# Kernel tuning notes

Hardware: AMD Instinct MI355X
Metric: run time of the kernel (lower is better)

## Reference

```python
import jax, jax.numpy as jnp
import numpy as np

H = 128          # hidden_dim
B = 4096         # number of graphs (segments)
N = 1048576      # total nodes
NUM_OBS = 1


def setup_inputs() -> dict:
    key = jax.random.key(0)
    ks = jax.random.split(key, 10)
    h = jax.random.normal(ks[0], (N, H), dtype=jnp.float32)
    batch = jnp.sort(jax.random.randint(ks[1], (N,), 0, B, dtype=jnp.int64))
    s = 1.0 / np.sqrt(H)
    s2 = 1.0 / np.sqrt(2 * H)
    # gate: Linear(H,H) -> tanh -> Linear(H,1)
    gate_w1 = jax.random.uniform(ks[2], (H, H), jnp.float32, -s, s)
    gate_b1 = jax.random.uniform(ks[3], (H,), jnp.float32, -s, s)
    gate_w2 = jax.random.uniform(ks[4], (H, 1), jnp.float32, -s, s)
    gate_b2 = jax.random.uniform(ks[5], (1,), jnp.float32, -s, s)
    # mlp: Linear(2H,H) -> ReLU -> Linear(H,num_obs)  (dropout off in eval)
    mlp_w1 = jax.random.uniform(ks[6], (2 * H, H), jnp.float32, -s2, s2)
    mlp_b1 = jax.random.uniform(ks[7], (H,), jnp.float32, -s2, s2)
    mlp_w2 = jax.random.uniform(ks[8], (H, NUM_OBS), jnp.float32, -s, s)
    mlp_b2 = jax.random.uniform(ks[9], (NUM_OBS,), jnp.float32, -s, s)
    return {"h": h, "batch": batch,
            "gate_w1": gate_w1, "gate_b1": gate_b1,
            "gate_w2": gate_w2, "gate_b2": gate_b2,
            "mlp_w1": mlp_w1, "mlp_b1": mlp_b1,
            "mlp_w2": mlp_w2, "mlp_b2": mlp_b2}


def reference(h, batch, gate_w1, gate_b1, gate_w2, gate_b2,
              mlp_w1, mlp_b1, mlp_w2, mlp_b2):
    # gate scores per node: (N,)
    score = (jnp.tanh(h @ gate_w1 + gate_b1) @ gate_w2 + gate_b2)[:, 0]
    # segment softmax over nodes of each graph (numerically stable)
    seg_max = jax.ops.segment_max(score, batch, num_segments=B)
    e = jnp.exp(score - seg_max[batch])
    seg_sum = jax.ops.segment_sum(e, batch, num_segments=B)
    attn = e / seg_sum[batch]                      # (N,)
    # attention-weighted sum pooling: (B, H)
    g_attn = jax.ops.segment_sum(h * attn[:, None], batch, num_segments=B)
    # max pooling: (B, H)
    g_max = jax.ops.segment_max(h, batch, num_segments=B)
    g = jnp.concatenate([g_attn, g_max], axis=-1)  # (B, 2H)
    hidden = jax.nn.relu(g @ mlp_w1 + mlp_b1)
    return hidden @ mlp_w2 + mlp_b2               # (B, NUM_OBS)
```

## Files before the change

### kernel.cpp

```cpp
#include <hip/hip_runtime.h>
#include <hip/hip_bf16.h>
#include <cfloat>

#define HD 128

typedef float f32x4 __attribute__((ext_vector_type(4)));
typedef __bf16 bf16x8 __attribute__((ext_vector_type(8)));

__global__ void seg_bounds_kernel(const int* __restrict__ batch, int n, int nseg,
                                  int* __restrict__ seg_start) {
  int b = blockIdx.x * blockDim.x + threadIdx.x;
  if (b > nseg) return;
  if (b == nseg) { seg_start[b] = n; return; }
  int lo = 0, hi = n;
  while (lo < hi) {
    int mid = (lo + hi) >> 1;
    if (batch[mid] < b) lo = mid + 1; else hi = mid;
  }
  seg_start[b] = lo;
}

template <int CTRL>
__device__ __forceinline__ float dpp_ror(float v) {
  return __int_as_float(__builtin_amdgcn_update_dpp(
      0, __float_as_int(v), CTRL, 0xF, 0xF, true));
}


#define LOAD_TILE(BUF, T)                                                   \
  {                                                                         \
    const int nIt_ = (T) * 16 + lr;                                         \
    const size_t row_ = (size_t)s0 + (size_t)min(nIt_, lenm1);              \
    const float* hp_ = h + row_ * HD + 8 * kl;                              \
    _Pragma("unroll")                                                       \
    for (int kt = 0; kt < 4; ++kt) {                                        \
      *reinterpret_cast<float4*>(&BUF[8 * kt]) =                            \
          *reinterpret_cast<const float4*>(hp_ + 32 * kt);                  \
      *reinterpret_cast<float4*>(&BUF[8 * kt + 4]) =                        \
          *reinterpret_cast<const float4*>(hp_ + 32 * kt + 4);              \
    }                                                                       \
  }

#define PROC_TILE(BUF, T)                                                   \
  {                                                                         \
    const bool valid_ = ((T) * 16 + lr) < len;                              \
                 \
    asm volatile("" : "+v"(Cb));                                            \
    float p2_[4] = {0.f, 0.f, 0.f, 0.f};                                    \
    _Pragma("unroll")                                                       \
    for (int hf = 0; hf < 2; ++hf) {                                        \
      f32x4 macc_[4];                                                       \
      _Pragma("unroll")                                                     \
      for (int fh = 0; fh < 4; ++fh) macc_[fh] = (f32x4){0.f, 0.f, 0.f, 0.f}; \
      __builtin_amdgcn_s_setprio(1);                                        \
      _Pragma("unroll")                                                     \
      for (int kt = 0; kt < 4; ++kt) {                                      \
        bf16x8 acur_;                                                       \
        _Pragma("unroll")                                                   \
        for (int j = 0; j < 8; ++j) acur_[j] = (__bf16)BUF[8 * kt + j];     \
        const char* bp_ = reinterpret_cast<const char*>(sWt) +              \
                          (Cb + ((kt ^ hi2) << 6)) + hf * 16384;            \
        bf16x8 bfr_[4];                                                     \
        _Pragma("unroll")                                                   \
        for (int fh = 0; fh < 4; ++fh)                                      \
          bfr_[fh] = *reinterpret_cast<const bf16x8*>(bp_ + fh * 4096);     \
        _Pragma("unroll")                                                   \
        for (int fh = 0; fh < 4; ++fh)                                      \
          macc_[fh] = __builtin_amdgcn_mfma_f32_16x16x32_bf16(              \
              acur_, bfr_[fh], macc_[fh], 0, 0, 0);                         \
      }                                                                     \
      __builtin_amdgcn_s_setprio(0);                                        \
      _Pragma("unroll")                                                     \
      for (int fh = 0; fh < 4; ++fh) {                                      \
        const int f_ = 4 * hf + fh;                                         \
        _Pragma("unroll")                                                   \
        for (int r = 0; r < 4; ++r) {                                       \
          const float xe_ = fmaf(LOG2E2, macc_[fh][r], b1s[f_]);            \
          const float e_ = exp2f(xe_);                                      \
          const float t_ = __builtin_amdgcn_rcpf(1.f + e_);                 \
          p2_[r] = fmaf(t_, w2r[f_], p2_[r]);                               \
        }                                                                   \
      }                                                                     \
    }                                                                       \
               \
    _Pragma("unroll")                                                       \
    for (int r = 0; r < 4; ++r) {                                           \
      p2_[r] += dpp_ror<0x121>(p2_[r]);                                     \
      p2_[r] += dpp_ror<0x122>(p2_[r]);                                     \
      p2_[r] += dpp_ror<0x124>(p2_[r]);                                     \
      p2_[r] += dpp_ror<0x128>(p2_[r]);                                     \
    }                                                                       \
    const int rr_ = lr & 3;                                                 \
    const float psel_ =                                                     \
        rr_ == 0 ? p2_[0] : (rr_ == 1 ? p2_[1] : (rr_ == 2 ? p2_[2]         \
                                                            : p2_[3]));     \
    const float sc_ = __shfl(psel_, ((lr >> 2) << 4) | (lr & 3), 64);       \
    const float w_ = valid_ ? exp2f(sc_ * NEG2LOG2E) : 0.f;                 \
    s += w_;                                                                \
    _Pragma("unroll")                                                       \
    for (int j = 0; j < 32; ++j) {                                          \
      acc[j] = fmaf(BUF[j], w_, acc[j]);                                    \
      gm[j] = fmaxf(gm[j], BUF[j]);                                         \
    }                                                                       \
  }

__global__ __launch_bounds__(256, 2) void fused_pool_kernel(
    const float* __restrict__ h, const float* __restrict__ w1,
    const float* __restrict__ b1, const float* __restrict__ w2,
    const int* __restrict__ seg_start, int B,
    const float* __restrict__ w1m, const float* __restrict__ b1m,
    const float* __restrict__ w2m, const float* __restrict__ b2m,
    float* __restrict__ out)
{
  __shared__ __bf16 sWt[HD * HD];
  __shared__ float sG[4][256];

  for (int i = threadIdx.x; i < HD * HD / 4; i += 256) {
    const int k = i >> 5;
    const int c4 = (i & 31) << 2;
    const float4 v = reinterpret_cast<const float4*>(w1)[i];
    const float vv[4] = {v.x, v.y, v.z, v.w};
#pragma unroll
    for (int q = 0; q < 4; ++q) {
      const int c = c4 + q;
      sWt[c * HD + ((((k >> 3) ^ (c & 15)) << 3) | (k & 7))] = (__bf16)vv[q];
    }
  }
  __syncthreads();

  const float LOG2E2    = 2.88539008177792681f;
  const float NEG2LOG2E = -2.88539008177792681f;

  const int lane = threadIdx.x & 63;
  const int wid  = threadIdx.x >> 6;
  const int lr   = lane & 15;
  const int kl   = lane >> 4;

  float w2r[8], b1s[8];
#pragma unroll
  for (int f = 0; f < 8; ++f) {
    w2r[f] = w2[16 * f + lr];
    b1s[f] = LOG2E2 * b1[16 * f + lr];
  }

  const int hi2 = (lr >> 2) & 3;
  int Cb = lr * 256 + ((kl ^ (lr & 3)) << 4);

  const int segStride = gridDim.x * 4;
  for (int b = blockIdx.x * 4 + wid; b < B; b += segStride) {
    const int s0  = seg_start[b];
    const int len = seg_start[b + 1] - s0;
    const int lenm1 = len - 1;
    const int nt  = (len + 15) >> 4;

    float s = 0.f;
    float acc[32], gm[32];
#pragma unroll
    for (int j = 0; j < 32; ++j) { acc[j] = 0.f; gm[j] = -FLT_MAX; }

    if (nt > 0) {
      float hA[32], hB[32];
      LOAD_TILE(hA, 0)
      LOAD_TILE(hB, 1)
      for (int t = 0; t < nt; t += 2) {
        PROC_TILE(hA, t)
        LOAD_TILE(hA, t + 2)
        PROC_TILE(hB, t + 1)
        LOAD_TILE(hB, t + 3)
      }
    }

#pragma unroll
    for (int st = 1; st <= 8; st <<= 1) {
      if (st == 1) {
        s += dpp_ror<0x121>(s);
#pragma unroll
        for (int j = 0; j < 32; ++j) {
          acc[j] += dpp_ror<0x121>(acc[j]);
          gm[j] = fmaxf(gm[j], dpp_ror<0x121>(gm[j]));
        }
      } else if (st == 2) {
        s += dpp_ror<0x122>(s);
#pragma unroll
        for (int j = 0; j < 32; ++j) {
          acc[j] += dpp_ror<0x122>(acc[j]);
          gm[j] = fmaxf(gm[j], dpp_ror<0x122>(gm[j]));
        }
      } else if (st == 4) {
        s += dpp_ror<0x124>(s);
#pragma unroll
        for (int j = 0; j < 32; ++j) {
          acc[j] += dpp_ror<0x124>(acc[j]);
          gm[j] = fmaxf(gm[j], dpp_ror<0x124>(gm[j]));
        }
      } else {
        s += dpp_ror<0x128>(s);
#pragma unroll
        for (int j = 0; j < 32; ++j) {
          acc[j] += dpp_ror<0x128>(acc[j]);
          gm[j] = fmaxf(gm[j], dpp_ror<0x128>(gm[j]));
        }
      }
    }

    if (lr == 0) {
      const float invS = (s > 0.f) ? 1.f / s : 0.f;
#pragma unroll
      for (int kt = 0; kt < 4; ++kt) {
        const int fb = 32 * kt + 8 * kl;
        float4 va, vb, ma, mb;
        va.x = acc[8*kt+0]*invS; va.y = acc[8*kt+1]*invS;
        va.z = acc[8*kt+2]*invS; va.w = acc[8*kt+3]*invS;
        vb.x = acc[8*kt+4]*invS; vb.y = acc[8*kt+5]*invS;
        vb.z = acc[8*kt+6]*invS; vb.w = acc[8*kt+7]*invS;
        ma.x = gm[8*kt+0]; ma.y = gm[8*kt+1]; ma.z = gm[8*kt+2]; ma.w = gm[8*kt+3];
        mb.x = gm[8*kt+4]; mb.y = gm[8*kt+5]; mb.z = gm[8*kt+6]; mb.w = gm[8*kt+7];
        *reinterpret_cast<float4*>(&sG[wid][fb])           = va;
        *reinterpret_cast<float4*>(&sG[wid][fb + 4])       = vb;
        *reinterpret_cast<float4*>(&sG[wid][128 + fb])     = ma;
        *reinterpret_cast<float4*>(&sG[wid][128 + fb + 4]) = mb;
      }
    }
    asm volatile("s_waitcnt lgkmcnt(0)" ::: "memory");

    {
      const int u = lane;
      float a0 = b1m[u], a1 = b1m[u + 64];
      const float* wp0 = w1m + u;
#pragma unroll 8
      for (int kq = 0; kq < 64; ++kq) {
        const float4 g4 = *reinterpret_cast<const float4*>(&sG[wid][4 * kq]);
        const float* wk = wp0 + (size_t)(4 * kq) * HD;
        a0 = fmaf(g4.x, wk[0],            a0);
        a1 = fmaf(g4.x, wk[64],           a1);
        a0 = fmaf(g4.y, wk[HD],           a0);
        a1 = fmaf(g4.y, wk[HD + 64],      a1);
        a0 = fmaf(g4.z, wk[2 * HD],       a0);
        a1 = fmaf(g4.z, wk[2 * HD + 64],  a1);
        a0 = fmaf(g4.w, wk[3 * HD],       a0);
        a1 = fmaf(g4.w, wk[3 * HD + 64],  a1);
      }
      float v = fmaxf(a0, 0.f) * w2m[u] + fmaxf(a1, 0.f) * w2m[u + 64];
#pragma unroll
      for (int off = 32; off >= 1; off >>= 1) v += __shfl_xor(v, off, 64);
      if (lane == 0) out[b] = v + b2m[0];
    }
  }
}

extern "C" void kernel_launch(void* const* d_in, const int* in_sizes, int n_in,
                              void* d_out, int out_size, void* d_ws, size_t ws_size,
                              hipStream_t stream) {
  const float* h       = (const float*)d_in[0];
  const int*   batch   = (const int*)d_in[1];
  const float* gate_w1 = (const float*)d_in[2];
  const float* gate_b1 = (const float*)d_in[3];
  const float* gate_w2 = (const float*)d_in[4];
  const float* mlp_w1  = (const float*)d_in[6];
  const float* mlp_b1  = (const float*)d_in[7];
  const float* mlp_w2  = (const float*)d_in[8];
  const float* mlp_b2  = (const float*)d_in[9];
  float* out = (float*)d_out;

  const int N = in_sizes[0] / HD;
  const int B = out_size;

  int* seg = (int*)d_ws;

  seg_bounds_kernel<<<(B + 256) / 256, 256, 0, stream>>>(batch, N, B, seg);
  fused_pool_kernel<<<1024, 256, 0, stream>>>(h, gate_w1, gate_b1, gate_w2,
                                              seg, B, mlp_w1, mlp_b1, mlp_w2,
                                              mlp_b2, out);
}
```

Baseline: 158.1 us.

## Triple-buffer node tiles as packed bf16 registers to deepen prefetch

Loads each 16-node tile into one fp32 staging buffer and immediately converts it to packed bf16 registers. This allows three tiles in flight (A/B/C rotation) instead of two fp32 buffers. The MFMA inputs, and also the attention-weighted sum and max pooling, now read the bf16 values. The goal is to cut register usage and hide more global-load latency, at the cost of reduced precision in the pooled outputs.

```diff
diff --git a/kernel.cpp b/kernel.cpp
--- a/kernel.cpp
+++ b/kernel.cpp
@@ -27,21 +27,32 @@
 }
 
 
-#define LOAD_TILE(BUF, T)                                                   \
+#define LOADF_TILE(T)                                                       \
   {                                                                         \
     const int nIt_ = (T) * 16 + lr;                                         \
     const size_t row_ = (size_t)s0 + (size_t)min(nIt_, lenm1);              \
     const float* hp_ = h + row_ * HD + 8 * kl;                              \
     _Pragma("unroll")                                                       \
     for (int kt = 0; kt < 4; ++kt) {                                        \
-      *reinterpret_cast<float4*>(&BUF[8 * kt]) =                            \
+      *reinterpret_cast<float4*>(&F[8 * kt]) =                              \
           *reinterpret_cast<const float4*>(hp_ + 32 * kt);                  \
-      *reinterpret_cast<float4*>(&BUF[8 * kt + 4]) =                        \
+      *reinterpret_cast<float4*>(&F[8 * kt + 4]) =                          \
           *reinterpret_cast<const float4*>(hp_ + 32 * kt + 4);              \
     }                                                                       \
   }
 
-#define PROC_TILE(BUF, T)                                                   \
+#define CVT_TILE(PK)                                                        \
+  {                                                                         \
+    _Pragma("unroll")                                                       \
+    for (int kt = 0; kt < 4; ++kt) {                                        \
+      bf16x8 p_;                                                            \
+      _Pragma("unroll")                                                     \
+      for (int j = 0; j < 8; ++j) p_[j] = (__bf16)F[8 * kt + j];            \
+      PK[kt] = p_;                                                          \
+    }                                                                       \
+  }
+
+#define PROC_TILE(PK, T)                                                    \
   {                                                                         \
     const bool valid_ = ((T) * 16 + lr) < len;                              \
                  \
@@ -55,9 +66,6 @@
       __builtin_amdgcn_s_setprio(1);                                        \
       _Pragma("unroll")                                                     \
       for (int kt = 0; kt < 4; ++kt) {                                      \
-        bf16x8 acur_;                                                       \
-        _Pragma("unroll")                                                   \
-        for (int j = 0; j < 8; ++j) acur_[j] = (__bf16)BUF[8 * kt + j];     \
         const char* bp_ = reinterpret_cast<const char*>(sWt) +              \
                           (Cb + ((kt ^ hi2) << 6)) + hf * 16384;            \
         bf16x8 bfr_[4];                                                     \
@@ -67,7 +75,7 @@
         _Pragma("unroll")                                                   \
         for (int fh = 0; fh < 4; ++fh)                                      \
           macc_[fh] = __builtin_amdgcn_mfma_f32_16x16x32_bf16(              \
-              acur_, bfr_[fh], macc_[fh], 0, 0, 0);                         \
+              PK[kt], bfr_[fh], macc_[fh], 0, 0, 0);                        \
       }                                                                     \
       __builtin_amdgcn_s_setprio(0);                                        \
       _Pragma("unroll")                                                     \
@@ -98,9 +106,13 @@
     const float w_ = valid_ ? exp2f(sc_ * NEG2LOG2E) : 0.f;                 \
     s += w_;                                                                \
     _Pragma("unroll")                                                       \
-    for (int j = 0; j < 32; ++j) {                                          \
-      acc[j] = fmaf(BUF[j], w_, acc[j]);                                    \
-      gm[j] = fmaxf(gm[j], BUF[j]);                                         \
+    for (int kt = 0; kt < 4; ++kt) {                                        \
+      _Pragma("unroll")                                                     \
+      for (int j = 0; j < 8; ++j) {                                         \
+        const float hv_ = (float)PK[kt][j];            \
+        acc[8 * kt + j] = fmaf(hv_, w_, acc[8 * kt + j]);                   \
+        gm[8 * kt + j] = fmaxf(gm[8 * kt + j], hv_);                        \
+      }                                                                     \
     }                                                                       \
   }
 
@@ -159,14 +171,21 @@
     for (int j = 0; j < 32; ++j) { acc[j] = 0.f; gm[j] = -FLT_MAX; }
 
     if (nt > 0) {
-      float hA[32], hB[32];
-      LOAD_TILE(hA, 0)
-      LOAD_TILE(hB, 1)
-      for (int t = 0; t < nt; t += 2) {
+      float F[32];
+      bf16x8 hA[4], hB[4], hC[4];
+      LOADF_TILE(0) CVT_TILE(hA)
+      LOADF_TILE(1) CVT_TILE(hB)
+      LOADF_TILE(2)
+      for (int t = 0; t < nt; t += 3) {
+        CVT_TILE(hC)
+        LOADF_TILE(t + 3)
         PROC_TILE(hA, t)
-        LOAD_TILE(hA, t + 2)
+        CVT_TILE(hA)
+        LOADF_TILE(t + 4)
         PROC_TILE(hB, t + 1)
-        LOAD_TILE(hB, t + 3)
+        CVT_TILE(hB)
+        LOADF_TILE(t + 5)
+        PROC_TILE(hC, t + 2)
       }
     }
 
```

Measured after the change: 355.0 us. +124.5%, slower.

## Stage h tiles into LDS via async global_load_lds with 4-deep ring

Applied to the files above, without the earlier changes.

Replaces the register double-buffered h loads with direct global-to-LDS async copies into a four-slot per-wave ring, prefetching four tiles ahead. The gate weight matrix is now held in registers (Bf fragments), so it no longer has to be read from LDS on every tile, which frees LDS for the staging buffers. Blocks shrink to 2 waves with 64KB of dynamic LDS and one block per CU, which lowers occupancy in exchange for deeper per-wave prefetch. The vmcnt/lgkmcnt bookkeeping is hand-tuned and fragile, and the large register footprint of the held weights may cause spills.

```diff
diff --git a/kernel.cpp b/kernel.cpp
--- a/kernel.cpp
+++ b/kernel.cpp
@@ -27,25 +27,47 @@
 }
 
 
-#define LOAD_TILE(BUF, T)                                                   \
+#define STAGE_TILE(T, SLOT)                                                 \
   {                                                                         \
-    const int nIt_ = (T) * 16 + lr;                                         \
-    const size_t row_ = (size_t)s0 + (size_t)min(nIt_, lenm1);              \
-    const float* hp_ = h + row_ * HD + 8 * kl;                              \
-    _Pragma("unroll")                                                       \
-    for (int kt = 0; kt < 4; ++kt) {                                        \
-      *reinterpret_cast<float4*>(&BUF[8 * kt]) =                            \
-          *reinterpret_cast<const float4*>(hp_ + 32 * kt);                  \
-      *reinterpret_cast<float4*>(&BUF[8 * kt + 4]) =                        \
-          *reinterpret_cast<const float4*>(hp_ + 32 * kt + 4);              \
-    }                                                                       \
-  }
-
-#define PROC_TILE(BUF, T)                                                   \
+    _Pragma("unroll")                                                       \
+    for (int j_ = 0; j_ < 8; ++j_) {                                        \
+      const int rj_ = 2 * j_ + (lane >> 5);                                 \
+      const int grow_ = s0 + min((T) * 16 + rj_, lenm1);                    \
+      const float* gp_ =                                                    \
+          h + (size_t)grow_ * HD + (((lane & 31) ^ rj_) << 2);              \
+      __builtin_amdgcn_global_load_lds(                                     \
+          gp_, (void*)(dynLds + wid * 32768 + (SLOT) * 8192 + j_ * 1024),   \
+          16, 0, 0);                                                        \
+    }                                                                       \
+  }
+
+#define PROC_TILE(T)                                                        \
   {                                                                         \
     const bool valid_ = ((T) * 16 + lr) < len;                              \
-                 \
-    asm volatile("" : "+v"(Cb));                                            \
+    const char* tb_ = dynLds + wid * 32768 + ((T) & 3) * 8192 + lr * 512;   \
+    float hv_[32];                                                          \
+    bf16x8 aq_[4];                                                          \
+    _Pragma("unroll")                                                       \
+    for (int kt = 0; kt < 4; ++kt) {                                        \
+      const int q0_ = (8 * kt + 2 * kl) ^ lr;                               \
+      const float4 v0_ = *reinterpret_cast<const float4*>(tb_ + q0_ * 16);  \
+      const float4 v1_ =                                                    \
+          *reinterpret_cast<const float4*>(tb_ + (q0_ ^ 1) * 16);           \
+      hv_[8*kt+0] = v0_.x; hv_[8*kt+1] = v0_.y;                             \
+      hv_[8*kt+2] = v0_.z; hv_[8*kt+3] = v0_.w;                             \
+      hv_[8*kt+4] = v1_.x; hv_[8*kt+5] = v1_.y;                             \
+      hv_[8*kt+6] = v1_.z; hv_[8*kt+7] = v1_.w;                             \
+      bf16x8 a_;                                                            \
+      a_[0] = (__bf16)v0_.x; a_[1] = (__bf16)v0_.y;                         \
+      a_[2] = (__bf16)v0_.z; a_[3] = (__bf16)v0_.w;                         \
+      a_[4] = (__bf16)v1_.x; a_[5] = (__bf16)v1_.y;                         \
+      a_[6] = (__bf16)v1_.z; a_[7] = (__bf16)v1_.w;                         \
+      aq_[kt] = a_;                                                         \
+    }                                                                       \
+       \
+                               \
+    asm volatile("s_waitcnt lgkmcnt(0)" ::: "memory");                      \
+    STAGE_TILE((T) + 4, (T) & 3)                                            \
     float p2_[4] = {0.f, 0.f, 0.f, 0.f};                                    \
     _Pragma("unroll")                                                       \
     for (int hf = 0; hf < 2; ++hf) {                                        \
@@ -55,19 +77,10 @@
       __builtin_amdgcn_s_setprio(1);                                        \
       _Pragma("unroll")                                                     \
       for (int kt = 0; kt < 4; ++kt) {                                      \
-        bf16x8 acur_;                                                       \
-        _Pragma("unroll")                                                   \
-        for (int j = 0; j < 8; ++j) acur_[j] = (__bf16)BUF[8 * kt + j];     \
-        const char* bp_ = reinterpret_cast<const char*>(sWt) +              \
-                          (Cb + ((kt ^ hi2) << 6)) + hf * 16384;            \
-        bf16x8 bfr_[4];                                                     \
-        _Pragma("unroll")                                                   \
-        for (int fh = 0; fh < 4; ++fh)                                      \
-          bfr_[fh] = *reinterpret_cast<const bf16x8*>(bp_ + fh * 4096);     \
         _Pragma("unroll")                                                   \
         for (int fh = 0; fh < 4; ++fh)                                      \
           macc_[fh] = __builtin_amdgcn_mfma_f32_16x16x32_bf16(              \
-              acur_, bfr_[fh], macc_[fh], 0, 0, 0);                         \
+              aq_[kt], Bf[4 * hf + fh][kt], macc_[fh], 0, 0, 0);            \
       }                                                                     \
       __builtin_amdgcn_s_setprio(0);                                        \
       _Pragma("unroll")                                                     \
@@ -82,7 +95,6 @@
         }                                                                   \
       }                                                                     \
     }                                                                       \
-               \
     _Pragma("unroll")                                                       \
     for (int r = 0; r < 4; ++r) {                                           \
       p2_[r] += dpp_ror<0x121>(p2_[r]);                                     \
@@ -99,12 +111,12 @@
     s += w_;                                                                \
     _Pragma("unroll")                                                       \
     for (int j = 0; j < 32; ++j) {                                          \
-      acc[j] = fmaf(BUF[j], w_, acc[j]);                                    \
-      gm[j] = fmaxf(gm[j], BUF[j]);                                         \
-    }                                                                       \
-  }
-
-__global__ __launch_bounds__(256, 2) void fused_pool_kernel(
+      acc[j] = fmaf(hv_[j], w_, acc[j]);                                    \
+      gm[j] = fmaxf(gm[j], hv_[j]);                                         \
+    }                                                                       \
+  }
+
+__global__ __launch_bounds__(128, 1) void fused_pool_kernel(
     const float* __restrict__ h, const float* __restrict__ w1,
     const float* __restrict__ b1, const float* __restrict__ w2,
     const int* __restrict__ seg_start, int B,
@@ -112,29 +124,38 @@
     const float* __restrict__ w2m, const float* __restrict__ b2m,
     float* __restrict__ out)
 {
-  __shared__ __bf16 sWt[HD * HD];
-  __shared__ float sG[4][256];
-
-  for (int i = threadIdx.x; i < HD * HD / 4; i += 256) {
-    const int k = i >> 5;
-    const int c4 = (i & 31) << 2;
-    const float4 v = reinterpret_cast<const float4*>(w1)[i];
-    const float vv[4] = {v.x, v.y, v.z, v.w};
-#pragma unroll
-    for (int q = 0; q < 4; ++q) {
-      const int c = c4 + q;
-      sWt[c * HD + ((((k >> 3) ^ (c & 15)) << 3) | (k & 7))] = (__bf16)vv[q];
-    }
-  }
+  extern __shared__ __align__(16) char dynLds[];
+
+  const int tid  = threadIdx.x;
+  const int lane = tid & 63;
+  const int wid  = tid >> 6;
+  const int lr   = lane & 15;
+  const int kl   = lane >> 4;
+
+  {
+    __bf16* sWt = reinterpret_cast<__bf16*>(dynLds);
+    for (int i = tid; i < HD * HD / 4; i += 128) {
+      const int k = i >> 5;
+      const int c4 = (i & 31) << 2;
+      const float4 v = reinterpret_cast<const float4*>(w1)[i];
+      const float vv[4] = {v.x, v.y, v.z, v.w};
+#pragma unroll
+      for (int q = 0; q < 4; ++q) sWt[(c4 + q) * HD + k] = (__bf16)vv[q];
+    }
+  }
+  __syncthreads();
+  bf16x8 Bf[8][4];
+#pragma unroll
+  for (int f = 0; f < 8; ++f)
+#pragma unroll
+    for (int kt = 0; kt < 4; ++kt)
+      Bf[f][kt] = *reinterpret_cast<const bf16x8*>(
+          reinterpret_cast<const __bf16*>(dynLds) +
+          (16 * f + lr) * HD + 32 * kt + 8 * kl);
   __syncthreads();
 
   const float LOG2E2    = 2.88539008177792681f;
   const float NEG2LOG2E = -2.88539008177792681f;
-
-  const int lane = threadIdx.x & 63;
-  const int wid  = threadIdx.x >> 6;
-  const int lr   = lane & 15;
-  const int kl   = lane >> 4;
 
   float w2r[8], b1s[8];
 #pragma unroll
@@ -143,11 +164,7 @@
     b1s[f] = LOG2E2 * b1[16 * f + lr];
   }
 
-  const int hi2 = (lr >> 2) & 3;
-  int Cb = lr * 256 + ((kl ^ (lr & 3)) << 4);
-
-  const int segStride = gridDim.x * 4;
-  for (int b = blockIdx.x * 4 + wid; b < B; b += segStride) {
+  for (int b = blockIdx.x * 2 + wid; b < B; b += gridDim.x * 2) {
     const int s0  = seg_start[b];
     const int len = seg_start[b + 1] - s0;
     const int lenm1 = len - 1;
@@ -159,14 +176,13 @@
     for (int j = 0; j < 32; ++j) { acc[j] = 0.f; gm[j] = -FLT_MAX; }
 
     if (nt > 0) {
-      float hA[32], hB[32];
-      LOAD_TILE(hA, 0)
-      LOAD_TILE(hB, 1)
-      for (int t = 0; t < nt; t += 2) {
-        PROC_TILE(hA, t)
-        LOAD_TILE(hA, t + 2)
-        PROC_TILE(hB, t + 1)
-        LOAD_TILE(hB, t + 3)
+      STAGE_TILE(0, 0)
+      STAGE_TILE(1, 1)
+      STAGE_TILE(2, 2)
+      STAGE_TILE(3, 3)
+      for (int t = 0; t < nt; ++t) {
+        asm volatile("s_waitcnt vmcnt(24)" ::: "memory");
+        PROC_TILE(t)
       }
     }
 
@@ -202,6 +218,9 @@
         }
       }
     }
+
+    asm volatile("s_waitcnt vmcnt(0)" ::: "memory");
+    float* sG = reinterpret_cast<float*>(dynLds + wid * 32768);
 
     if (lr == 0) {
       const float invS = (s > 0.f) ? 1.f / s : 0.f;
@@ -215,10 +234,10 @@
         vb.z = acc[8*kt+6]*invS; vb.w = acc[8*kt+7]*invS;
         ma.x = gm[8*kt+0]; ma.y = gm[8*kt+1]; ma.z = gm[8*kt+2]; ma.w = gm[8*kt+3];
         mb.x = gm[8*kt+4]; mb.y = gm[8*kt+5]; mb.z = gm[8*kt+6]; mb.w = gm[8*kt+7];
-        *reinterpret_cast<float4*>(&sG[wid][fb])           = va;
-        *reinterpret_cast<float4*>(&sG[wid][fb + 4])       = vb;
-        *reinterpret_cast<float4*>(&sG[wid][128 + fb])     = ma;
-        *reinterpret_cast<float4*>(&sG[wid][128 + fb + 4]) = mb;
+        *reinterpret_cast<float4*>(&sG[fb])           = va;
+        *reinterpret_cast<float4*>(&sG[fb + 4])       = vb;
+        *reinterpret_cast<float4*>(&sG[128 + fb])     = ma;
+        *reinterpret_cast<float4*>(&sG[128 + fb + 4]) = mb;
       }
     }
     asm volatile("s_waitcnt lgkmcnt(0)" ::: "memory");
@@ -229,7 +248,7 @@
       const float* wp0 = w1m + u;
 #pragma unroll 8
       for (int kq = 0; kq < 64; ++kq) {
-        const float4 g4 = *reinterpret_cast<const float4*>(&sG[wid][4 * kq]);
+        const float4 g4 = *reinterpret_cast<const float4*>(&sG[4 * kq]);
         const float* wk = wp0 + (size_t)(4 * kq) * HD;
         a0 = fmaf(g4.x, wk[0],            a0);
         a1 = fmaf(g4.x, wk[64],           a1);
@@ -268,7 +287,7 @@
   int* seg = (int*)d_ws;
 
   seg_bounds_kernel<<<(B + 256) / 256, 256, 0, stream>>>(batch, N, B, seg);
-  fused_pool_kernel<<<1024, 256, 0, stream>>>(h, gate_w1, gate_b1, gate_w2,
-                                              seg, B, mlp_w1, mlp_b1, mlp_w2,
-                                              mlp_b2, out);
-}
+  fused_pool_kernel<<<1024, 128, 65536, stream>>>(h, gate_w1, gate_b1,
+                                                  gate_w2, seg, B, mlp_w1,
+                                                  mlp_b1, mlp_w2, mlp_b2, out);
+}
```

Measured after the change: 293.3 us. +85.5%, slower.
